# Performance work log

Measured on AMD Instinct MI355X. Metric: run time of the kernel, lower is better.

## Reference

```python
import jax, jax.numpy as jnp
import numpy as np

N, M, E = 14541, 237, 120000
XS, GS, HID, OUT, H = 100, 100, 100, 100, 2
NEG_SLOPE = 0.2


def _l2(v, axis):
    # F.normalize(p=2): x / clamp_min(||x||, 1e-12)
    return v / jnp.maximum(jnp.linalg.norm(v, axis=axis, keepdims=True), 1e-12)


def _rel_att(h_ijk, ends, n, W, b, w_att, out):
    # edge MLP -> [E, H, out]
    c = (h_ijk @ W.T + b).reshape(-1, H, out)
    # attention logits per edge/head, b_ijk = -leaky_relu(a_ijk)
    a = jnp.sum(w_att * c, axis=2, keepdims=True)            # [E, H, 1]
    e = jnp.exp(-jax.nn.leaky_relu(a, NEG_SLOPE))            # [E, H, 1]
    denom = jax.ops.segment_sum(e, ends, num_segments=n)     # [n, H, 1]
    alpha = e / denom[ends]                                  # scatter-softmax
    # self zero-edges in original == segment_sum zero-init; elu(0)=0 matches
    h = jax.ops.segment_sum(alpha * c, ends, num_segments=n) # [n, H, out]
    return jax.nn.elu(h)


def setup_inputs() -> dict:
    key = jax.random.key(0)
    ks = jax.random.split(key, 24)
    f32 = jnp.float32
    def w(k, shp, s=0.1):
        return jax.random.normal(k, shp, dtype=f32) * s
    inp = {
        "x": jax.random.normal(ks[0], (N, XS), dtype=f32),
        "g": jax.random.normal(ks[1], (M, GS), dtype=f32),
        # layer-1 inbound/outbound attention (fc1: [H*HID, 2*XS+GS])
        "W1in": w(ks[2], (H * HID, 2 * XS + GS)), "b1in": jnp.zeros((H * HID,), f32), "a1in": w(ks[3], (1, H, HID)),
        "W1out": w(ks[4], (H * HID, 2 * XS + GS)), "b1out": jnp.zeros((H * HID,), f32), "a1out": w(ks[5], (1, H, HID)),
        "Wa1": w(ks[6], (1, 2 * HID)), "ba1": jnp.zeros((1,), f32),
        # layer-2 attention (fc1: [H*OUT, 2*H*HID+GS])
        "W2in": w(ks[7], (H * OUT, 2 * H * HID + GS)), "b2in": jnp.zeros((H * OUT,), f32), "a2in": w(ks[8], (1, H, OUT)),
        "W2out": w(ks[9], (H * OUT, 2 * H * HID + GS)), "b2out": jnp.zeros((H * OUT,), f32), "a2out": w(ks[10], (1, H, OUT)),
        "Wa2": w(ks[11], (1, 2 * OUT)), "ba2": jnp.zeros((1,), f32),
        # entity residual projection and relation projection
        "Went": w(ks[12], (H * OUT, XS)), "bent": jnp.zeros((H * OUT,), f32),
        "Wrel": w(ks[13], (H * OUT, GS)), "brel": jnp.zeros((H * OUT,), f32),
        "edge_idx": jax.random.randint(ks[14], (2, E), 0, N),
        "edge_type": jax.random.randint(ks[15], (E,), 0, M),
    }
    return inp


def reference(x, g, W1in, b1in, a1in, W1out, b1out, a1out, Wa1, ba1,
              W2in, b2in, a2in, W2out, b2out, a2out, Wa2, ba2,
              Went, bent, Wrel, brel, edge_idx, edge_type):
    n = x.shape[0]
    xn = _l2(x, 1)
    row, col = edge_idx[0], edge_idx[1]
    # layer 1
    h_ijk = jnp.concatenate([xn[row], xn[col], g[edge_type]], axis=1)  # [E, 2*XS+GS]
    hin = _rel_att(h_ijk, col, n, W1in, b1in, a1in, HID)
    hout = _rel_att(h_ijk, row, n, W1out, b1out, a1out, HID)
    al = jax.nn.sigmoid(jnp.concatenate([hin, hout], axis=2) @ Wa1.T + ba1)  # [n, H, 1]
    h = al * hin + (1.0 - al) * hout
    h = _l2(jax.nn.elu(h), 2).reshape(n, H * HID)  # head-concat
    # layer 2
    h_ijk = jnp.concatenate([h[row], h[col], g[edge_type]], axis=1)  # [E, 2*H*HID+GS]
    hin = _rel_att(h_ijk, col, n, W2in, b2in, a2in, OUT)
    hout = _rel_att(h_ijk, row, n, W2out, b2out, a2out, OUT)
    al = jax.nn.sigmoid(jnp.concatenate([hin, hout], axis=2) @ Wa2.T + ba2)
    h = al * hin + (1.0 - al) * hout
    h = _l2(jax.nn.elu(h), 2)                       # [n, H, OUT]
    # entity residual + relation projection
    h_prime = (xn @ Went.T + bent).reshape(n, H, OUT) + h
    h_prime = _l2(h_prime, 2).reshape(n, H * OUT)
    g_prime = g @ Wrel.T + brel                     # [M, H*OUT]
    return h_prime, g_prime
```

## Files before the change

kernel.cpp:

```cpp
#include <hip/hip_runtime.h>
#include <math.h>

#define NSLOPE 0.2f

typedef unsigned short ushort_t;
typedef __attribute__((ext_vector_type(8))) short bf16x8;
typedef __attribute__((ext_vector_type(8))) unsigned short ushort8;
typedef __attribute__((ext_vector_type(4))) float f32x4;

__device__ __forceinline__ float elu1(float x) { return x > 0.f ? x : expm1f(x); }

__device__ __forceinline__ ushort_t f2bf(float f) {
  union { float f; unsigned int u; } v; v.f = f;
  unsigned int r = v.u + 0x7fffu + ((v.u >> 16) & 1u);
  return (ushort_t)(r >> 16);
}
__device__ __forceinline__ float bf2f(ushort_t u) {
  union { unsigned int i; float f; } v; v.i = ((unsigned int)u) << 16; return v.f;
}


__device__ void dev_build_w(int idx,
                            const float* __restrict__ W1in, const float* __restrict__ W1out,
                            const float* __restrict__ W2in, const float* __restrict__ W2out,
                            const float* __restrict__ Went,
                            ushort_t* __restrict__ wcat1, ushort_t* __restrict__ wcat2,
                            ushort_t* __restrict__ wentb) {
  const int S1 = 832 * 128, S2 = 832 * 256, S3 = 256 * 128;
  if (idx < S1) {
    int ro = idx >> 7, k = idx & 127;
    float val = 0.f;
    if (ro < 800 && k < 100) {
      int o = ro / 200, cc = ro - o * 200;
      const float* W = (o < 2) ? W1in : W1out;
      val = W[(size_t)cc * 300 + (o & 1) * 100 + k];
    }
    wcat1[idx] = f2bf(val);
  } else if (idx < S1 + S2) {
    int i2 = idx - S1;
    int ro = i2 >> 8, k = i2 & 255;
    float val = 0.f;
    if (ro < 800 && k < 200) {
      int o = ro / 200, cc = ro - o * 200;
      const float* W = (o < 2) ? W2in : W2out;
      val = W[(size_t)cc * 500 + (o & 1) * 200 + k];
    }
    wcat2[i2] = f2bf(val);
  } else if (idx < S1 + S2 + S3) {
    int i3 = idx - S1 - S2;
    int ro = i3 >> 7, k = i3 & 127;
    float val = (ro < 200 && k < 100) ? Went[ro * 100 + k] : 0.f;
    wentb[i3] = f2bf(val);
  }
}

__device__ void dev_makeu(int idx,
                          const float* __restrict__ W1in, const float* __restrict__ a1in,
                          const float* __restrict__ W1out, const float* __restrict__ a1out,
                          const float* __restrict__ W2in, const float* __restrict__ a2in,
                          const float* __restrict__ W2out, const float* __restrict__ a2out,
                          float* __restrict__ u1in, float* __restrict__ u1out,
                          float* __restrict__ u2in, float* __restrict__ u2out) {
  if (idx >= 3200) return;
  const float* W; const float* avec; float* u; int Kp, local;
  if (idx < 600)       { W = W1in;  avec = a1in;  u = u1in;  Kp = 300; local = idx; }
  else if (idx < 1200) { W = W1out; avec = a1out; u = u1out; Kp = 300; local = idx - 600; }
  else if (idx < 2200) { W = W2in;  avec = a2in;  u = u2in;  Kp = 500; local = idx - 1200; }
  else                 { W = W2out; avec = a2out; u = u2out; Kp = 500; local = idx - 2200; }
  int h = local / Kp, kp = local - h * Kp;
  const float* Wb = W + (size_t)(h * 100) * Kp + kp;
  const float* ab = avec + h * 100;
  float s = 0.f;
  for (int k = 0; k < 100; ++k) s += ab[k] * Wb[(size_t)k * Kp];
  u[local] = s;
}

__device__ void dev_l2norm_q(int bb, int tid, const float* __restrict__ x,
                             ushort_t* __restrict__ xnb,
                             const float* __restrict__ u1in, const float* __restrict__ u1out,
                             float* __restrict__ qA, float* __restrict__ qB,
                             float* __restrict__ qC, float* __restrict__ qD, int N) {
  int wid = bb * 4 + (tid >> 6);
  int lane = tid & 63;
  if (wid >= N) return;
  const float* p = x + (size_t)wid * 100;
  float v0 = p[lane];
  bool t2 = lane < 36;
  float v1 = t2 ? p[lane + 64] : 0.f;
  float ss = v0 * v0 + v1 * v1;
#pragma unroll
  for (int m = 1; m < 64; m <<= 1) ss += __shfl_xor(ss, m, 64);
  float inv = 1.f / fmaxf(sqrtf(ss), 1e-12f);
  float a0 = v0 * inv, a1 = v1 * inv;
  ushort_t* ob = xnb + (size_t)wid * 128;
  ob[lane] = f2bf(a0);
  ob[64 + lane] = t2 ? f2bf(a1) : (ushort_t)0;
  int k0 = lane, k1 = 64 + lane;
  float s[8];
  s[0] = a0 * u1in[k0]        + (t2 ? a1 * u1in[k1]        : 0.f);
  s[1] = a0 * u1in[300 + k0]  + (t2 ? a1 * u1in[300 + k1]  : 0.f);
  s[2] = a0 * u1in[100 + k0]  + (t2 ? a1 * u1in[100 + k1]  : 0.f);
  s[3] = a0 * u1in[400 + k0]  + (t2 ? a1 * u1in[400 + k1]  : 0.f);
  s[4] = a0 * u1out[k0]       + (t2 ? a1 * u1out[k1]       : 0.f);
  s[5] = a0 * u1out[300 + k0] + (t2 ? a1 * u1out[300 + k1] : 0.f);
  s[6] = a0 * u1out[100 + k0] + (t2 ? a1 * u1out[100 + k1] : 0.f);
  s[7] = a0 * u1out[400 + k0] + (t2 ? a1 * u1out[400 + k1] : 0.f);
#pragma unroll
  for (int m = 1; m < 64; m <<= 1) {
#pragma unroll
    for (int i = 0; i < 8; ++i) s[i] += __shfl_xor(s[i], m, 64);
  }
  if (lane == 0) {
    qA[wid * 2] = s[0]; qA[wid * 2 + 1] = s[1];
    qB[wid * 2] = s[2]; qB[wid * 2 + 1] = s[3];
    qC[wid * 2] = s[4]; qC[wid * 2 + 1] = s[5];
    qD[wid * 2] = s[6]; qD[wid * 2 + 1] = s[7];
  }
}

__device__ void dev_qrel2(int bb, int tid, const float* __restrict__ g,
                          const float* __restrict__ u1in, const float* __restrict__ u1out,
                          const float* __restrict__ u2in, const float* __restrict__ u2out,
                          float* __restrict__ q3i1, float* __restrict__ q3o1,
                          float* __restrict__ q3i2, float* __restrict__ q3o2, int Mn) {
  int wid = bb * 4 + (tid >> 6);
  int lane = tid & 63;
  if (wid >= 2 * Mn) return;
  int lay = wid >= Mn;
  int m = wid - lay * Mn;
  const float* uin  = lay ? u2in  : u1in;
  const float* uout = lay ? u2out : u1out;
  int Kp = lay ? 500 : 300;
  int off3 = lay ? 400 : 200;
  float* q3i = lay ? q3i2 : q3i1;
  float* q3o = lay ? q3o2 : q3o1;
  const float* a = g + (size_t)m * 100;
  float s[4] = {0.f, 0.f, 0.f, 0.f};
  for (int k = lane; k < 100; k += 64) {
    float av = a[k];
    s[0] += av * uin[off3 + k];
    s[1] += av * uin[Kp + off3 + k];
    s[2] += av * uout[off3 + k];
    s[3] += av * uout[Kp + off3 + k];
  }
#pragma unroll
  for (int mm = 1; mm < 64; mm <<= 1) {
#pragma unroll
    for (int i = 0; i < 4; ++i) s[i] += __shfl_xor(s[i], mm, 64);
  }
  if (lane == 0) {
    q3i[m * 2] = s[0]; q3i[m * 2 + 1] = s[1];
    q3o[m * 2] = s[2]; q3o[m * 2 + 1] = s[3];
  }
}

__device__ void dev_count(int bb, int tid, const int* __restrict__ row,
                          const int* __restrict__ col,
                          int* __restrict__ cntIn, int* __restrict__ cntOut, int E) {
  int e = bb * 256 + tid;
  if (e >= E) return;
  atomicAdd(&cntIn[col[e]], 1);
  atomicAdd(&cntOut[row[e]], 1);
}

__device__ void dev_edge_e(int bb, int tid,
                           const int* __restrict__ row, const int* __restrict__ col,
                           const int* __restrict__ ety,
                           const float* __restrict__ qA, const float* __restrict__ qB,
                           const float* __restrict__ q3i,
                           const float* __restrict__ qC, const float* __restrict__ qD,
                           const float* __restrict__ q3o,
                           const int* __restrict__ invIn, const int* __restrict__ invOut,
                           float2* __restrict__ eIc, float2* __restrict__ eOc, int E) {
  int e = bb * 256 + tid;
  if (e >= E) return;
  int r = row[e], c = col[e], t = ety[e];
  float2 vA = *(const float2*)(qA + (size_t)r * 2);
  float2 vB = *(const float2*)(qB + (size_t)c * 2);
  float2 v3 = *(const float2*)(q3i + (size_t)t * 2);
  float2 vC = *(const float2*)(qC + (size_t)r * 2);
  float2 vD = *(const float2*)(qD + (size_t)c * 2);
  float2 v4 = *(const float2*)(q3o + (size_t)t * 2);
  float a0 = vA.x + vB.x + v3.x, a1 = vA.y + vB.y + v3.y;
  float b0 = vC.x + vD.x + v4.x, b1 = vC.y + vD.y + v4.y;
  float2 rI, rO;
  rI.x = expf(-(a0 > 0.f ? a0 : NSLOPE * a0));
  rI.y = expf(-(a1 > 0.f ? a1 : NSLOPE * a1));
  rO.x = expf(-(b0 > 0.f ? b0 : NSLOPE * b0));
  rO.y = expf(-(b1 > 0.f ? b1 : NSLOPE * b1));
  eIc[invIn[e]] = rI;
  eOc[invOut[e]] = rO;
}

__device__ void dev_mfma(int bx, int by, int tid,
                         ushort_t* __restrict__ smA, ushort_t* __restrict__ smB,
                         const ushort_t* __restrict__ Ab, int lda,
                         const ushort_t* __restrict__ Bb, int Kpad,
                         int R, int NC, int OUTW, const float* __restrict__ bias,
                         float* __restrict__ C0,
                         ushort_t* __restrict__ Bd0, ushort_t* __restrict__ Bd1,
                         ushort_t* __restrict__ Bd2, ushort_t* __restrict__ Bd3) {
  const int lane = tid & 63;
  const int w = tid >> 6;
  const int wm = w >> 1, wn = w & 1;
  const int m0 = by * 64;
  const int n0 = bx * 64;
  const int srow = tid >> 2;
  const int sq = tid & 3;
  const int sw3 = srow & 7;
  const int sbase = srow * 64;
  const int so0 = sbase + ((((sq << 1) + 0) ^ sw3) << 3);
  const int so1 = sbase + ((((sq << 1) + 1) ^ sw3) << 3);
  const bool aok = (m0 + srow) < R;
  const ushort_t* Ag = Ab + (size_t)(m0 + srow) * lda + sq * 16;
  const ushort_t* Bg = Bb + (size_t)(n0 + srow) * Kpad + sq * 16;
  const int lswz = lane & 7;
  const int hi = lane >> 4;
  const int rA0 = (wm * 32 + (lane & 15)) * 64;
  const int rB0 = (wn * 32 + (lane & 15)) * 64;
  f32x4 acc[2][2] = {};
  for (int k0 = 0; k0 < Kpad; k0 += 64) {
    ushort8 a0 = {0, 0, 0, 0, 0, 0, 0, 0}, a1 = {0, 0, 0, 0, 0, 0, 0, 0};
    if (aok) {
      a0 = *(const ushort8*)(Ag + k0);
      a1 = *(const ushort8*)(Ag + k0 + 8);
    }
    ushort8 b0 = *(const ushort8*)(Bg + k0);
    ushort8 b1 = *(const ushort8*)(Bg + k0 + 8);
    __syncthreads();
    *(ushort8*)(smA + so0) = a0;
    *(ushort8*)(smA + so1) = a1;
    *(ushort8*)(smB + so0) = b0;
    *(ushort8*)(smB + so1) = b1;
    __syncthreads();
#pragma unroll
    for (int ks = 0; ks < 2; ++ks) {
      int co = (((ks << 2) + hi) ^ lswz) << 3;
      bf16x8 aA = *(const bf16x8*)(smA + rA0 + co);
      bf16x8 aB = *(const bf16x8*)(smA + rA0 + 1024 + co);
      bf16x8 bA = *(const bf16x8*)(smB + rB0 + co);
      bf16x8 bB = *(const bf16x8*)(smB + rB0 + 1024 + co);
      acc[0][0] = __builtin_amdgcn_mfma_f32_16x16x32_bf16(aA, bA, acc[0][0], 0, 0, 0);
      acc[0][1] = __builtin_amdgcn_mfma_f32_16x16x32_bf16(aA, bB, acc[0][1], 0, 0, 0);
      acc[1][0] = __builtin_amdgcn_mfma_f32_16x16x32_bf16(aB, bA, acc[1][0], 0, 0, 0);
      acc[1][1] = __builtin_amdgcn_mfma_f32_16x16x32_bf16(aB, bB, acc[1][1], 0, 0, 0);
    }
  }
  ushort_t* Bds[4] = {Bd0, Bd1, Bd2, Bd3};
#pragma unroll
  for (int mt = 0; mt < 2; ++mt) {
    int rr0 = m0 + wm * 32 + mt * 16 + (lane >> 4) * 4;
#pragma unroll
    for (int nt = 0; nt < 2; ++nt) {
      int cc = n0 + wn * 32 + nt * 16 + (lane & 15);
      if (cc < NC) {
        int o = cc / OUTW;
        int c2 = cc - o * OUTW;
        float bv = bias ? bias[c2] : 0.f;
        ushort_t* Bd = Bds[o];
        if (Bd) {
#pragma unroll
          for (int reg = 0; reg < 4; ++reg) {
            int r = rr0 + reg;
            if (r < R) Bd[(size_t)r * OUTW + c2] = f2bf(acc[mt][nt][reg] + bv);
          }
        } else {
#pragma unroll
          for (int reg = 0; reg < 4; ++reg) {
            int r = rr0 + reg;
            if (r < R) C0[(size_t)r * OUTW + c2] = acc[mt][nt][reg] + bv;
          }
        }
      }
    }
  }
}

template <int NOUT, int BF>
__device__ void dev_gemm_multi(int bx, int by, int tid, float4 (*As)[25],
                               const float* __restrict__ A, int lda,
                               const float* __restrict__ W0, const float* __restrict__ W1,
                               int ldw,
                               const float* __restrict__ b0, const float* __restrict__ b1,
                               void* __restrict__ C0v, void* __restrict__ C1v, int R) {
  const int K4 = 25;
  int row0 = by * 32;
  {
    int r = tid >> 3;
    int rr = row0 + r;
    const float4* Ar = (const float4*)(A + (size_t)rr * lda);
    for (int k4 = (tid & 7); k4 < K4; k4 += 8)
      As[r][k4] = (rr < R) ? Ar[k4] : make_float4(0.f, 0.f, 0.f, 0.f);
  }
  __syncthreads();
  int c = bx * 64 + (tid & 63);
  if (c < 200) {
    int rb = (tid >> 6) << 3;
    const float4* Wr[NOUT];
    Wr[0] = (const float4*)(W0 + (size_t)c * ldw);
    if (NOUT > 1) Wr[1] = (const float4*)(W1 + (size_t)c * ldw);
    float acc[NOUT][8];
#pragma unroll
    for (int o = 0; o < NOUT; ++o)
#pragma unroll
      for (int i = 0; i < 8; ++i) acc[o][i] = 0.f;
#pragma unroll 2
    for (int k4 = 0; k4 < K4; ++k4) {
      float4 a[8];
#pragma unroll
      for (int i = 0; i < 8; ++i) a[i] = As[rb + i][k4];
#pragma unroll
      for (int o = 0; o < NOUT; ++o) {
        float4 wv = Wr[o][k4];
#pragma unroll
        for (int i = 0; i < 8; ++i)
          acc[o][i] += a[i].x * wv.x + a[i].y * wv.y + a[i].z * wv.z + a[i].w * wv.w;
      }
    }
    float bv[NOUT];
    bv[0] = b0 ? b0[c] : 0.f;
    if (NOUT > 1) bv[1] = b1 ? b1[c] : 0.f;
    void* Cp[NOUT];
    Cp[0] = C0v;
    if (NOUT > 1) Cp[1] = C1v;
#pragma unroll
    for (int i = 0; i < 8; ++i) {
      int rr = row0 + rb + i;
      if (rr < R) {
#pragma unroll
        for (int o = 0; o < NOUT; ++o) {
          float val = acc[o][i] + bv[o];
          if (BF) ((ushort_t*)Cp[o])[(size_t)rr * 200 + c] = f2bf(val);
          else    ((float*)Cp[o])[(size_t)rr * 200 + c] = val;
        }
      }
    }
  }
}


__global__ __launch_bounds__(256) void MEGA0(
    const float* W1in, const float* W1out, const float* W2in, const float* W2out,
    const float* Went,
    ushort_t* wcat1, ushort_t* wcat2, ushort_t* wentb,
    const float* a1in, const float* a1out, const float* a2in, const float* a2out,
    float* u1in, float* u1out, float* u2in, float* u2out,
    int* cntIn, int* cntOut, int N, int nb_bw, int nb_mk) {
  int b = blockIdx.x, tid = threadIdx.x;
  if (b < nb_bw) {
    dev_build_w(b * 256 + tid, W1in, W1out, W2in, W2out, Went, wcat1, wcat2, wentb);
  } else if (b < nb_bw + nb_mk) {
    dev_makeu((b - nb_bw) * 256 + tid, W1in, a1in, W1out, a1out, W2in, a2in, W2out, a2out,
              u1in, u1out, u2in, u2out);
  } else {
    int idx = (b - nb_bw - nb_mk) * 256 + tid;
    if (idx < N) cntIn[idx] = 0;
    else if (idx < 2 * N) cntOut[idx - N] = 0;
  }
}

__global__ __launch_bounds__(256) void MEGA1(
    const float* x, ushort_t* xnb, const float* u1in, const float* u1out,
    float* qA, float* qB, float* qC, float* qD, int N,
    const float* g, const float* u2in, const float* u2out,
    float* q3i1, float* q3o1, float* q3i2, float* q3o2, int Mn,
    const int* row, const int* col, int* cntIn, int* cntOut, int E,
    int nb_l2, int nb_qr) {
  int b = blockIdx.x, tid = threadIdx.x;
  if (b < nb_l2) {
    dev_l2norm_q(b, tid, x, xnb, u1in, u1out, qA, qB, qC, qD, N);
  } else if (b < nb_l2 + nb_qr) {
    dev_qrel2(b - nb_l2, tid, g, u1in, u1out, u2in, u2out, q3i1, q3o1, q3i2, q3o2, Mn);
  } else {
    dev_count(b - nb_l2 - nb_qr, tid, row, col, cntIn, cntOut, E);
  }
}

__global__ __launch_bounds__(256) void k_scanA(const int* __restrict__ cntIn,
                                               const int* __restrict__ cntOut,
                                               int* __restrict__ part, int N, int nbc) {
  __shared__ int wsum[4];
  int b = blockIdx.x;
  const int* cnt = (b < nbc) ? cntIn : cntOut;
  int cb = (b < nbc) ? b : b - nbc;
  int idx = cb * 256 + threadIdx.x;
  int v = (idx < N) ? cnt[idx] : 0;
#pragma unroll
  for (int m = 1; m < 64; m <<= 1) v += __shfl_xor(v, m, 64);
  if ((threadIdx.x & 63) == 0) wsum[threadIdx.x >> 6] = v;
  __syncthreads();
  if (threadIdx.x == 0) part[b] = wsum[0] + wsum[1] + wsum[2] + wsum[3];
}

__global__ __launch_bounds__(256) void k_scanB(int* __restrict__ part,
                                               int* __restrict__ rsIn, int* __restrict__ rsOut,
                                               int nbc, int N) {
  __shared__ int buf[512];
  int t = threadIdx.x;
  buf[t]       = (t < nbc) ? part[t] : 0;
  buf[256 + t] = (t < nbc) ? part[nbc + t] : 0;
  __syncthreads();
  for (int off = 1; off < 256; off <<= 1) {
    int v0 = (t >= off) ? buf[t - off] : 0;
    int v1 = (t >= off) ? buf[256 + t - off] : 0;
    __syncthreads();
    buf[t] += v0; buf[256 + t] += v1;
    __syncthreads();
  }
  if (t < nbc) {
    part[t]       = (t == 0) ? 0 : buf[t - 1];
    part[nbc + t] = (t == 0) ? 0 : buf[256 + t - 1];
  }
  if (t == 0) { rsIn[N] = buf[nbc - 1]; rsOut[N] = buf[256 + nbc - 1]; }
}

__global__ __launch_bounds__(256) void k_scanC(const int* __restrict__ cntIn,
                                               const int* __restrict__ cntOut,
                                               const int* __restrict__ part,
                                               int* __restrict__ rsIn, int* __restrict__ rsOut,
                                               int* __restrict__ posIn, int* __restrict__ posOut,
                                               int N, int nbc) {
  __shared__ int buf[256];
  int b = blockIdx.x;
  const int* cnt = (b < nbc) ? cntIn : cntOut;
  int* rs  = (b < nbc) ? rsIn : rsOut;
  int* pos = (b < nbc) ? posIn : posOut;
  int cb = (b < nbc) ? b : b - nbc;
  int base = part[b];
  int t = threadIdx.x;
  int idx = cb * 256 + t;
  buf[t] = (idx < N) ? cnt[idx] : 0;
  __syncthreads();
  for (int off = 1; off < 256; off <<= 1) {
    int v = (t >= off) ? buf[t - off] : 0;
    __syncthreads();
    buf[t] += v;
    __syncthreads();
  }
  if (idx < N) {
    int excl = base + ((t == 0) ? 0 : buf[t - 1]);
    rs[idx] = excl; pos[idx] = excl;
  }
}

__global__ void k_fill(const int* __restrict__ row, const int* __restrict__ col,
                       const int* __restrict__ ety,
                       int* __restrict__ posIn, int* __restrict__ posOut,
                       int2* __restrict__ pinIn, int2* __restrict__ pinOut,
                       int* __restrict__ invIn, int* __restrict__ invOut, int E) {
  int e = blockIdx.x * blockDim.x + threadIdx.x;
  if (e >= E) return;
  int r = row[e], c = col[e], tt = ety[e];
  int p = atomicAdd(&posIn[c], 1);
  pinIn[p] = make_int2(r, tt);
  invIn[e] = p;
  int q = atomicAdd(&posOut[r], 1);
  pinOut[q] = make_int2(c, tt);
  invOut[e] = q;
}

__global__ __launch_bounds__(256) void MEGA2(
    const ushort_t* xnb, const ushort_t* wcat1,
    ushort_t* PAb, ushort_t* PBb, ushort_t* PCb, ushort_t* PDb, int N,
    const int* row, const int* col, const int* ety,
    const float* qA, const float* qB, const float* q3i1,
    const float* qC, const float* qD, const float* q3o1,
    const int* invIn, const int* invOut, float2* eIc, float2* eOc, int E,
    const float* g, const float* W1in200, const float* W1out200,
    const float* b1in, const float* b1out, ushort_t* P3ib, ushort_t* P3ob, int Mn,
    const ushort_t* wentb, const float* bent, float* hent,
    const float* Wrel, const float* brel, float* outg,
    int nb_mf, int nb_ee, int nb_gm, int nb_we) {
  __shared__ float4 shbuf4[1024];
  ushort_t* smA = (ushort_t*)shbuf4;
  ushort_t* smB = smA + 64 * 64;
  float4 (*As)[25] = (float4(*)[25])shbuf4;
  int b = blockIdx.x, tid = threadIdx.x;
  if (b < nb_mf) {
    dev_mfma(b % 13, b / 13, tid, smA, smB, xnb, 128, wcat1, 128, N, 800, 200, nullptr,
             nullptr, PAb, PBb, PCb, PDb);
  } else if ((b -= nb_mf) < nb_ee) {
    dev_edge_e(b, tid, row, col, ety, qA, qB, q3i1, qC, qD, q3o1,
               invIn, invOut, eIc, eOc, E);
  } else if ((b -= nb_ee) < nb_gm) {
    dev_gemm_multi<2, 1>(b & 3, b >> 2, tid, As, g, 100, W1in200, W1out200, 300,
                         b1in, b1out, P3ib, P3ob, Mn);
  } else if ((b -= nb_gm) < nb_we) {
    dev_mfma(b & 3, b >> 2, tid, smA, smB, xnb, 128, wentb, 128, N, 200, 200, bent,
             hent, nullptr, nullptr, nullptr, nullptr);
  } else {
    b -= nb_we;
    dev_gemm_multi<1, 0>(b & 3, b >> 2, tid, As, g, 100, Wrel, nullptr, 100,
                         brel, nullptr, outg, nullptr, Mn);
  }
}

__global__ __launch_bounds__(256) void MEGA3(
    const ushort_t* h1b, const ushort_t* wcat2,
    ushort_t* PAb, ushort_t* PBb, ushort_t* PCb, ushort_t* PDb, int N,
    const int* row, const int* col, const int* ety,
    const float* qA, const float* qB, const float* q3i2,
    const float* qC, const float* qD, const float* q3o2,
    const int* invIn, const int* invOut, float2* eIc, float2* eOc, int E,
    const float* g, const float* W2in400, const float* W2out400,
    const float* b2in, const float* b2out, ushort_t* P3ib, ushort_t* P3ob, int Mn,
    int nb_mf, int nb_ee) {
  __shared__ float4 shbuf4[1024];
  ushort_t* smA = (ushort_t*)shbuf4;
  ushort_t* smB = smA + 64 * 64;
  float4 (*As)[25] = (float4(*)[25])shbuf4;
  int b = blockIdx.x, tid = threadIdx.x;
  if (b < nb_mf) {
    dev_mfma(b % 13, b / 13, tid, smA, smB, h1b, 256, wcat2, 256, N, 800, 200, nullptr,
             nullptr, PAb, PBb, PCb, PDb);
  } else if ((b -= nb_mf) < nb_ee) {
    dev_edge_e(b, tid, row, col, ety, qA, qB, q3i2, qC, qD, q3o2,
               invIn, invOut, eIc, eOc, E);
  } else {
    b -= nb_ee;
    dev_gemm_multi<2, 1>(b & 3, b >> 2, tid, As, g, 100, W2in400, W2out400, 500,
                         b2in, b2out, P3ib, P3ob, Mn);
  }
}

__global__ void k_node_att(const int2* __restrict__ pinIn, const float2* __restrict__ eIc,
                           const int* __restrict__ rsIn,
                           const int2* __restrict__ pinOut, const float2* __restrict__ eOc,
                           const int* __restrict__ rsOut,
                           const ushort_t* __restrict__ PAb, const ushort_t* __restrict__ PBb,
                           const ushort_t* __restrict__ PCb, const ushort_t* __restrict__ PDb,
                           const ushort_t* __restrict__ P3ib, const ushort_t* __restrict__ P3ob,
                           const float* __restrict__ Wg, const float* __restrict__ bg,
                           const float* __restrict__ u2in, const float* __restrict__ u2out,
                           float* __restrict__ qA, float* __restrict__ qB,
                           float* __restrict__ qC, float* __restrict__ qD,
                           ushort_t* __restrict__ Hb,
                           const float* __restrict__ hent, float* __restrict__ outp, int N) {
  int wid  = (int)((blockIdx.x * (unsigned)blockDim.x + threadIdx.x) >> 6);
  int lane = threadIdx.x & 63;
  if (wid >= N) return;
  int n = wid;
  int half = lane >> 5, i = lane & 31;
  bool act = i < 25;
  int j = half * 100 + i * 4;
  int sIn = rsIn[n], degIn = rsIn[n + 1] - sIn;
  int sOut = rsOut[n], degOut = rsOut[n + 1] - sOut;
  float4 accIn = {0.f, 0.f, 0.f, 0.f}, accOut = {0.f, 0.f, 0.f, 0.f};
  float dI0 = 0.f, dI1 = 0.f, dO0 = 0.f, dO1 = 0.f;
  int mx = max(degIn, degOut);
  for (int b = 0; b < mx; b += 64) {
    int l = b + lane;
    float2 evI = {0.f, 0.f}, evO = {0.f, 0.f};
    int2 ptI = {0, 0}, ptO = {0, 0};
    if (l < degIn)  { evI = eIc[sIn + l];  ptI = pinIn[sIn + l]; }
    if (l < degOut) { evO = eOc[sOut + l]; ptO = pinOut[sOut + l]; }
    dI0 += evI.x; dI1 += evI.y; dO0 += evO.x; dO1 += evO.y;
    int mI = degIn - b;  if (mI > 64) mI = 64;
    int mO = degOut - b; if (mO > 64) mO = 64;
    int m2 = max(mI, mO);
    for (int jj = 0; jj < m2; ++jj) {
      float aI0 = __shfl(evI.x, jj, 64), aI1 = __shfl(evI.y, jj, 64);
      int rI = __shfl(ptI.x, jj, 64), tI = __shfl(ptI.y, jj, 64);
      float aO0 = __shfl(evO.x, jj, 64), aO1 = __shfl(evO.y, jj, 64);
      int rO = __shfl(ptO.x, jj, 64), tO = __shfl(ptO.y, jj, 64);
      if (act && jj < mI) {
        float wgt = half ? aI1 : aI0;
        ushort4 pa = *(const ushort4*)(PAb + (size_t)rI * 200 + j);
        ushort4 p3 = *(const ushort4*)(P3ib + (size_t)tI * 200 + j);
        accIn.x += wgt * (bf2f(pa.x) + bf2f(p3.x));
        accIn.y += wgt * (bf2f(pa.y) + bf2f(p3.y));
        accIn.z += wgt * (bf2f(pa.z) + bf2f(p3.z));
        accIn.w += wgt * (bf2f(pa.w) + bf2f(p3.w));
      }
      if (act && jj < mO) {
        float wgt = half ? aO1 : aO0;
        ushort4 pd = *(const ushort4*)(PDb + (size_t)rO * 200 + j);
        ushort4 p3 = *(const ushort4*)(P3ob + (size_t)tO * 200 + j);
        accOut.x += wgt * (bf2f(pd.x) + bf2f(p3.x));
        accOut.y += wgt * (bf2f(pd.y) + bf2f(p3.y));
        accOut.z += wgt * (bf2f(pd.z) + bf2f(p3.z));
        accOut.w += wgt * (bf2f(pd.w) + bf2f(p3.w));
      }
    }
  }
#pragma unroll
  for (int m = 1; m < 64; m <<= 1) {
    dI0 += __shfl_xor(dI0, m, 64); dI1 += __shfl_xor(dI1, m, 64);
    dO0 += __shfl_xor(dO0, m, 64); dO1 += __shfl_xor(dO1, m, 64);
  }
  float4 hin = {0.f, 0.f, 0.f, 0.f}, hout = {0.f, 0.f, 0.f, 0.f};
  if (degIn > 0 && act) {
    float invd = 1.f / (half ? dI1 : dI0);
    ushort4 ps = *(const ushort4*)(PBb + (size_t)n * 200 + j);
    hin.x = elu1(bf2f(ps.x) + accIn.x * invd);
    hin.y = elu1(bf2f(ps.y) + accIn.y * invd);
    hin.z = elu1(bf2f(ps.z) + accIn.z * invd);
    hin.w = elu1(bf2f(ps.w) + accIn.w * invd);
  }
  if (degOut > 0 && act) {
    float invd = 1.f / (half ? dO1 : dO0);
    ushort4 ps = *(const ushort4*)(PCb + (size_t)n * 200 + j);
    hout.x = elu1(bf2f(ps.x) + accOut.x * invd);
    hout.y = elu1(bf2f(ps.y) + accOut.y * invd);
    hout.z = elu1(bf2f(ps.z) + accOut.z * invd);
    hout.w = elu1(bf2f(ps.w) + accOut.w * invd);
  }
  float gp = 0.f;
  if (act) {
    int k = i * 4;
    gp = Wg[k] * hin.x + Wg[k + 1] * hin.y + Wg[k + 2] * hin.z + Wg[k + 3] * hin.w +
         Wg[100 + k] * hout.x + Wg[100 + k + 1] * hout.y +
         Wg[100 + k + 2] * hout.z + Wg[100 + k + 3] * hout.w;
  }
#pragma unroll
  for (int m = 1; m < 32; m <<= 1) gp += __shfl_xor(gp, m, 32);
  float al = 1.f / (1.f + expf(-(gp + bg[0])));
  float4 he;
  he.x = elu1(al * hin.x + (1.f - al) * hout.x);
  he.y = elu1(al * hin.y + (1.f - al) * hout.y);
  he.z = elu1(al * hin.z + (1.f - al) * hout.z);
  he.w = elu1(al * hin.w + (1.f - al) * hout.w);
  float ss = he.x * he.x + he.y * he.y + he.z * he.z + he.w * he.w;
#pragma unroll
  for (int m = 1; m < 32; m <<= 1) ss += __shfl_xor(ss, m, 32);
  float inv = 1.f / fmaxf(sqrtf(ss), 1e-12f);
  float4 o = {he.x * inv, he.y * inv, he.z * inv, he.w * inv};
  if (Hb) {
    if (act) {
      ushort4 ov; ov.x = f2bf(o.x); ov.y = f2bf(o.y); ov.z = f2bf(o.z); ov.w = f2bf(o.w);
      *(ushort4*)(Hb + (size_t)n * 256 + j) = ov;
    } else {
      int pi = half * 7 + (i - 25);
      ushort4 z = {0, 0, 0, 0};
      *(ushort4*)(Hb + (size_t)n * 256 + 200 + pi * 4) = z;
    }
  }
  if (outp) {
    float4 v = {0.f, 0.f, 0.f, 0.f};
    if (act) {
      float4 hv = *(const float4*)(hent + (size_t)n * 200 + j);
      v.x = hv.x + o.x; v.y = hv.y + o.y; v.z = hv.z + o.z; v.w = hv.w + o.w;
    }
    float s2 = v.x * v.x + v.y * v.y + v.z * v.z + v.w * v.w;
#pragma unroll
    for (int m = 1; m < 32; m <<= 1) s2 += __shfl_xor(s2, m, 32);
    float inv2 = 1.f / fmaxf(sqrtf(s2), 1e-12f);
    if (act) {
      float4 ov = {v.x * inv2, v.y * inv2, v.z * inv2, v.w * inv2};
      *(float4*)(outp + (size_t)n * 200 + j) = ov;
    }
  }
  if (u2in) {
    float4 ov = act ? o : make_float4(0.f, 0.f, 0.f, 0.f);
    float s[8];
#pragma unroll
    for (int h = 0; h < 2; ++h) {
      float4 uA = *(const float4*)(u2in + h * 500 + j);
      float4 uB = *(const float4*)(u2in + h * 500 + 200 + j);
      float4 uC = *(const float4*)(u2out + h * 500 + j);
      float4 uD = *(const float4*)(u2out + h * 500 + 200 + j);
      s[0 + h] = ov.x * uA.x + ov.y * uA.y + ov.z * uA.z + ov.w * uA.w;
      s[2 + h] = ov.x * uB.x + ov.y * uB.y + ov.z * uB.z + ov.w * uB.w;
      s[4 + h] = ov.x * uC.x + ov.y * uC.y + ov.z * uC.z + ov.w * uC.w;
      s[6 + h] = ov.x * uD.x + ov.y * uD.y + ov.z * uD.z + ov.w * uD.w;
    }
#pragma unroll
    for (int m = 1; m < 64; m <<= 1) {
#pragma unroll
      for (int ii = 0; ii < 8; ++ii) s[ii] += __shfl_xor(s[ii], m, 64);
    }
    if (lane == 0) {
      qA[n * 2] = s[0]; qA[n * 2 + 1] = s[1];
      qB[n * 2] = s[2]; qB[n * 2 + 1] = s[3];
      qC[n * 2] = s[4]; qC[n * 2 + 1] = s[5];
      qD[n * 2] = s[6]; qD[n * 2 + 1] = s[7];
    }
  }
}

extern "C" void kernel_launch(void* const* d_in, const int* in_sizes, int n_in,
                              void* d_out, int out_size, void* d_ws, size_t ws_size,
                              hipStream_t stream) {
  const float* x    = (const float*)d_in[0];
  const float* g    = (const float*)d_in[1];
  const float* W1in = (const float*)d_in[2];
  const float* b1in = (const float*)d_in[3];
  const float* a1in = (const float*)d_in[4];
  const float* W1out= (const float*)d_in[5];
  const float* b1out= (const float*)d_in[6];
  const float* a1out= (const float*)d_in[7];
  const float* Wa1  = (const float*)d_in[8];
  const float* ba1  = (const float*)d_in[9];
  const float* W2in = (const float*)d_in[10];
  const float* b2in = (const float*)d_in[11];
  const float* a2in = (const float*)d_in[12];
  const float* W2out= (const float*)d_in[13];
  const float* b2out= (const float*)d_in[14];
  const float* a2out= (const float*)d_in[15];
  const float* Wa2  = (const float*)d_in[16];
  const float* ba2  = (const float*)d_in[17];
  const float* Went = (const float*)d_in[18];
  const float* bent = (const float*)d_in[19];
  const float* Wrel = (const float*)d_in[20];
  const float* brel = (const float*)d_in[21];
  const int*  eidx  = (const int*)d_in[22];
  const int*  ety   = (const int*)d_in[23];

  const int N = in_sizes[0] / 100;
  const int M = in_sizes[1] / 100;
  const int E = in_sizes[23];
  const int* row = eidx;
  const int* col = eidx + E;
  float* out = (float*)d_out;

  float* ws = (float*)d_ws;
  size_t off = 0;
  auto alloc = [&](size_t nf) { float* p = ws + off; off += (nf + 3) & ~(size_t)3; return p; };
  ushort_t* PAb = (ushort_t*)alloc((size_t)N * 100);
  ushort_t* PBb = (ushort_t*)alloc((size_t)N * 100);
  ushort_t* PCb = (ushort_t*)alloc((size_t)N * 100);
  ushort_t* PDb = (ushort_t*)alloc((size_t)N * 100);
  ushort_t* P3ib = (ushort_t*)alloc((size_t)M * 100);
  ushort_t* P3ob = (ushort_t*)alloc((size_t)M * 100);
  ushort_t* xnb = (ushort_t*)alloc((size_t)N * 64);
  ushort_t* h1b = (ushort_t*)alloc((size_t)N * 128);
  ushort_t* wcat1 = (ushort_t*)alloc((size_t)832 * 64);
  ushort_t* wcat2 = (ushort_t*)alloc((size_t)832 * 128);
  ushort_t* wentb = (ushort_t*)alloc((size_t)256 * 64);
  float* qA  = alloc((size_t)N * 2);
  float* qB  = alloc((size_t)N * 2);
  float* qC  = alloc((size_t)N * 2);
  float* qD  = alloc((size_t)N * 2);
  float* q3i1 = alloc((size_t)M * 2);
  float* q3o1 = alloc((size_t)M * 2);
  float* q3i2 = alloc((size_t)M * 2);
  float* q3o2 = alloc((size_t)M * 2);
  float2* eIc = (float2*)alloc((size_t)E * 2);
  float2* eOc = (float2*)alloc((size_t)E * 2);
  int2* pinIn  = (int2*)alloc((size_t)E * 2);
  int2* pinOut = (int2*)alloc((size_t)E * 2);
  int* invIn  = (int*)alloc((size_t)E);
  int* invOut = (int*)alloc((size_t)E);
  float* hent = alloc((size_t)N * 200);
  float* u1in  = alloc(600);
  float* u1out = alloc(600);
  float* u2in  = alloc(1000);
  float* u2out = alloc(1000);
  int* cntIn  = (int*)alloc((size_t)N);
  int* cntOut = (int*)alloc((size_t)N);
  int* rsIn   = (int*)alloc((size_t)N + 1);
  int* rsOut  = (int*)alloc((size_t)N + 1);
  int* posIn  = (int*)alloc((size_t)N);
  int* posOut = (int*)alloc((size_t)N);
  int* part   = (int*)alloc((size_t)512);

  const int gN4 = (N + 3) / 4;
  const int gE  = (E + 255) / 256;
  const int mT  = (N + 63) / 64;
  const int nbc = (N + 255) / 256;

  const int nb_bw = (832 * 128 + 832 * 256 + 256 * 128 + 255) / 256;
  const int nb_mk = 13;
  const int nb_z  = (2 * N + 255) / 256;
  const int nb_l2 = gN4;
  const int nb_qr = (2 * M + 3) / 4;
  const int nb_mf = 13 * mT;
  const int nb_gm = 4 * ((M + 31) / 32);
  const int nb_we = 4 * mT;

  MEGA0<<<nb_bw + nb_mk + nb_z, 256, 0, stream>>>(
      W1in, W1out, W2in, W2out, Went, wcat1, wcat2, wentb,
      a1in, a1out, a2in, a2out, u1in, u1out, u2in, u2out,
      cntIn, cntOut, N, nb_bw, nb_mk);

  MEGA1<<<nb_l2 + nb_qr + gE, 256, 0, stream>>>(
      x, xnb, u1in, u1out, qA, qB, qC, qD, N,
      g, u2in, u2out, q3i1, q3o1, q3i2, q3o2, M,
      row, col, cntIn, cntOut, E, nb_l2, nb_qr);

  k_scanA<<<2 * nbc, 256, 0, stream>>>(cntIn, cntOut, part, N, nbc);
  k_scanB<<<1, 256, 0, stream>>>(part, rsIn, rsOut, nbc, N);
  k_scanC<<<2 * nbc, 256, 0, stream>>>(cntIn, cntOut, part, rsIn, rsOut, posIn, posOut, N, nbc);
  k_fill<<<gE, 256, 0, stream>>>(row, col, ety, posIn, posOut, pinIn, pinOut, invIn, invOut, E);

  MEGA2<<<nb_mf + gE + nb_gm + nb_we + nb_gm, 256, 0, stream>>>(
      xnb, wcat1, PAb, PBb, PCb, PDb, N,
      row, col, ety, qA, qB, q3i1, qC, qD, q3o1, invIn, invOut, eIc, eOc, E,
      g, W1in + 200, W1out + 200, b1in, b1out, P3ib, P3ob, M,
      wentb, bent, hent, Wrel, brel, out + (size_t)N * 200,
      nb_mf, gE, nb_gm, nb_we);

  k_node_att<<<gN4, 256, 0, stream>>>(pinIn, eIc, rsIn, pinOut, eOc, rsOut,
                                      PAb, PBb, PCb, PDb, P3ib, P3ob, Wa1, ba1,
                                      u2in, u2out, qA, qB, qC, qD,
                                      h1b, nullptr, nullptr, N);

  MEGA3<<<nb_mf + gE + nb_gm, 256, 0, stream>>>(
      h1b, wcat2, PAb, PBb, PCb, PDb, N,
      row, col, ety, qA, qB, q3i2, qC, qD, q3o2, invIn, invOut, eIc, eOc, E,
      g, W2in + 400, W2out + 400, b2in, b2out, P3ib, P3ob, M,
      nb_mf, gE);

  k_node_att<<<gN4, 256, 0, stream>>>(pinIn, eIc, rsIn, pinOut, eOc, rsOut,
                                      PAb, PBb, PCb, PDb, P3ib, P3ob, Wa2, ba2,
                                      nullptr, nullptr, qA, qB, qC, qD,
                                      nullptr, hent, out, N);
}
```

Measured before the change: 200.3 us.

## Pack edge weights with CSR indices, stage them in LDS, move layer-2 relation GEMM earlier

Edge exp-weights and CSR (neighbor, type) pairs now share one interleaved float4 record per edge. The node-attention kernel reads a single 16-byte record per edge and stages records in shared memory, replacing eight wave shuffles per neighbor. The layer-2 relation GEMM moves into the earlier mega-kernel so MEGA3 holds only MFMA and edge work. The entity residual projection is stored as bf16 instead of fp32, halving that traffic at some cost in precision.

```diff
diff --git a/kernel.cpp b/kernel.cpp
--- a/kernel.cpp
+++ b/kernel.cpp
@@ -171,7 +171,7 @@
                            const float* __restrict__ qC, const float* __restrict__ qD,
                            const float* __restrict__ q3o,
                            const int* __restrict__ invIn, const int* __restrict__ invOut,
-                           float2* __restrict__ eIc, float2* __restrict__ eOc, int E) {
+                           float4* __restrict__ recI, float4* __restrict__ recO, int E) {
   int e = bb * 256 + tid;
   if (e >= E) return;
   int r = row[e], c = col[e], t = ety[e];
@@ -188,8 +188,8 @@
   rI.y = expf(-(a1 > 0.f ? a1 : NSLOPE * a1));
   rO.x = expf(-(b0 > 0.f ? b0 : NSLOPE * b0));
   rO.y = expf(-(b1 > 0.f ? b1 : NSLOPE * b1));
-  eIc[invIn[e]] = rI;
-  eOc[invOut[e]] = rO;
+  *(float2*)(recI + invIn[e]) = rI;
+  *(float2*)(recO + invOut[e]) = rO;
 }
 
 __device__ void dev_mfma(int bx, int by, int tid,
@@ -446,16 +446,16 @@
 __global__ void k_fill(const int* __restrict__ row, const int* __restrict__ col,
                        const int* __restrict__ ety,
                        int* __restrict__ posIn, int* __restrict__ posOut,
-                       int2* __restrict__ pinIn, int2* __restrict__ pinOut,
+                       float4* __restrict__ recI, float4* __restrict__ recO,
                        int* __restrict__ invIn, int* __restrict__ invOut, int E) {
   int e = blockIdx.x * blockDim.x + threadIdx.x;
   if (e >= E) return;
   int r = row[e], c = col[e], tt = ety[e];
   int p = atomicAdd(&posIn[c], 1);
-  pinIn[p] = make_int2(r, tt);
+  ((int2*)(recI + p))[1] = make_int2(r, tt);
   invIn[e] = p;
   int q = atomicAdd(&posOut[r], 1);
-  pinOut[q] = make_int2(c, tt);
+  ((int2*)(recO + q))[1] = make_int2(c, tt);
   invOut[e] = q;
 }
 
@@ -465,10 +465,12 @@
     const int* row, const int* col, const int* ety,
     const float* qA, const float* qB, const float* q3i1,
     const float* qC, const float* qD, const float* q3o1,
-    const int* invIn, const int* invOut, float2* eIc, float2* eOc, int E,
+    const int* invIn, const int* invOut, float4* recI, float4* recO, int E,
     const float* g, const float* W1in200, const float* W1out200,
-    const float* b1in, const float* b1out, ushort_t* P3ib, ushort_t* P3ob, int Mn,
-    const ushort_t* wentb, const float* bent, float* hent,
+    const float* b1in, const float* b1out, ushort_t* P3ib, ushort_t* P3ob,
+    const float* W2in400, const float* W2out400,
+    const float* b2in, const float* b2out, ushort_t* P3ib2, ushort_t* P3ob2, int Mn,
+    const ushort_t* wentb, const float* bent, ushort_t* hentb,
     const float* Wrel, const float* brel, float* outg,
     int nb_mf, int nb_ee, int nb_gm, int nb_we) {
   __shared__ float4 shbuf4[1024];
@@ -481,13 +483,16 @@
              nullptr, PAb, PBb, PCb, PDb);
   } else if ((b -= nb_mf) < nb_ee) {
     dev_edge_e(b, tid, row, col, ety, qA, qB, q3i1, qC, qD, q3o1,
-               invIn, invOut, eIc, eOc, E);
+               invIn, invOut, recI, recO, E);
   } else if ((b -= nb_ee) < nb_gm) {
     dev_gemm_multi<2, 1>(b & 3, b >> 2, tid, As, g, 100, W1in200, W1out200, 300,
                          b1in, b1out, P3ib, P3ob, Mn);
+  } else if ((b -= nb_gm) < nb_gm) {
+    dev_gemm_multi<2, 1>(b & 3, b >> 2, tid, As, g, 100, W2in400, W2out400, 500,
+                         b2in, b2out, P3ib2, P3ob2, Mn);
   } else if ((b -= nb_gm) < nb_we) {
     dev_mfma(b & 3, b >> 2, tid, smA, smB, xnb, 128, wentb, 128, N, 200, 200, bent,
-             hent, nullptr, nullptr, nullptr, nullptr);
+             nullptr, hentb, nullptr, nullptr, nullptr);
   } else {
     b -= nb_we;
     dev_gemm_multi<1, 0>(b & 3, b >> 2, tid, As, g, 100, Wrel, nullptr, 100,
@@ -501,32 +506,23 @@
     const int* row, const int* col, const int* ety,
     const float* qA, const float* qB, const float* q3i2,
     const float* qC, const float* qD, const float* q3o2,
-    const int* invIn, const int* invOut, float2* eIc, float2* eOc, int E,
-    const float* g, const float* W2in400, const float* W2out400,
-    const float* b2in, const float* b2out, ushort_t* P3ib, ushort_t* P3ob, int Mn,
-    int nb_mf, int nb_ee) {
+    const int* invIn, const int* invOut, float4* recI, float4* recO, int E,
+    int nb_mf) {
   __shared__ float4 shbuf4[1024];
   ushort_t* smA = (ushort_t*)shbuf4;
   ushort_t* smB = smA + 64 * 64;
-  float4 (*As)[25] = (float4(*)[25])shbuf4;
   int b = blockIdx.x, tid = threadIdx.x;
   if (b < nb_mf) {
     dev_mfma(b % 13, b / 13, tid, smA, smB, h1b, 256, wcat2, 256, N, 800, 200, nullptr,
              nullptr, PAb, PBb, PCb, PDb);
-  } else if ((b -= nb_mf) < nb_ee) {
-    dev_edge_e(b, tid, row, col, ety, qA, qB, q3i2, qC, qD, q3o2,
-               invIn, invOut, eIc, eOc, E);
   } else {
-    b -= nb_ee;
-    dev_gemm_multi<2, 1>(b & 3, b >> 2, tid, As, g, 100, W2in400, W2out400, 500,
-                         b2in, b2out, P3ib, P3ob, Mn);
-  }
-}
-
-__global__ void k_node_att(const int2* __restrict__ pinIn, const float2* __restrict__ eIc,
-                           const int* __restrict__ rsIn,
-                           const int2* __restrict__ pinOut, const float2* __restrict__ eOc,
-                           const int* __restrict__ rsOut,
+    dev_edge_e(b - nb_mf, tid, row, col, ety, qA, qB, q3i2, qC, qD, q3o2,
+               invIn, invOut, recI, recO, E);
+  }
+}
+
+__global__ void k_node_att(const float4* __restrict__ recI, const int* __restrict__ rsIn,
+                           const float4* __restrict__ recO, const int* __restrict__ rsOut,
                            const ushort_t* __restrict__ PAb, const ushort_t* __restrict__ PBb,
                            const ushort_t* __restrict__ PCb, const ushort_t* __restrict__ PDb,
                            const ushort_t* __restrict__ P3ib, const ushort_t* __restrict__ P3ob,
@@ -535,7 +531,10 @@
                            float* __restrict__ qA, float* __restrict__ qB,
                            float* __restrict__ qC, float* __restrict__ qD,
                            ushort_t* __restrict__ Hb,
-                           const float* __restrict__ hent, float* __restrict__ outp, int N) {
+                           const ushort_t* __restrict__ hentb, float* __restrict__ outp, int N) {
+  __shared__ float4 sRecI[4][64];
+  __shared__ float4 sRecO[4][64];
+  int wv = threadIdx.x >> 6;
   int wid  = (int)((blockIdx.x * (unsigned)blockDim.x + threadIdx.x) >> 6);
   int lane = threadIdx.x & 63;
   if (wid >= N) return;
@@ -550,21 +549,24 @@
   int mx = max(degIn, degOut);
   for (int b = 0; b < mx; b += 64) {
     int l = b + lane;
-    float2 evI = {0.f, 0.f}, evO = {0.f, 0.f};
-    int2 ptI = {0, 0}, ptO = {0, 0};
-    if (l < degIn)  { evI = eIc[sIn + l];  ptI = pinIn[sIn + l]; }
-    if (l < degOut) { evO = eOc[sOut + l]; ptO = pinOut[sOut + l]; }
-    dI0 += evI.x; dI1 += evI.y; dO0 += evO.x; dO1 += evO.y;
+    if (l < degIn) {
+      float4 rc = recI[sIn + l];
+      dI0 += rc.x; dI1 += rc.y;
+      sRecI[wv][lane] = rc;
+    }
+    if (l < degOut) {
+      float4 rc = recO[sOut + l];
+      dO0 += rc.x; dO1 += rc.y;
+      sRecO[wv][lane] = rc;
+    }
     int mI = degIn - b;  if (mI > 64) mI = 64;
     int mO = degOut - b; if (mO > 64) mO = 64;
     int m2 = max(mI, mO);
     for (int jj = 0; jj < m2; ++jj) {
-      float aI0 = __shfl(evI.x, jj, 64), aI1 = __shfl(evI.y, jj, 64);
-      int rI = __shfl(ptI.x, jj, 64), tI = __shfl(ptI.y, jj, 64);
-      float aO0 = __shfl(evO.x, jj, 64), aO1 = __shfl(evO.y, jj, 64);
-      int rO = __shfl(ptO.x, jj, 64), tO = __shfl(ptO.y, jj, 64);
       if (act && jj < mI) {
-        float wgt = half ? aI1 : aI0;
+        float4 rc = sRecI[wv][jj];
+        int rI = __float_as_int(rc.z), tI = __float_as_int(rc.w);
+        float wgt = half ? rc.y : rc.x;
         ushort4 pa = *(const ushort4*)(PAb + (size_t)rI * 200 + j);
         ushort4 p3 = *(const ushort4*)(P3ib + (size_t)tI * 200 + j);
         accIn.x += wgt * (bf2f(pa.x) + bf2f(p3.x));
@@ -573,7 +575,9 @@
         accIn.w += wgt * (bf2f(pa.w) + bf2f(p3.w));
       }
       if (act && jj < mO) {
-        float wgt = half ? aO1 : aO0;
+        float4 rc = sRecO[wv][jj];
+        int rO = __float_as_int(rc.z), tO = __float_as_int(rc.w);
+        float wgt = half ? rc.y : rc.x;
         ushort4 pd = *(const ushort4*)(PDb + (size_t)rO * 200 + j);
         ushort4 p3 = *(const ushort4*)(P3ob + (size_t)tO * 200 + j);
         accOut.x += wgt * (bf2f(pd.x) + bf2f(p3.x));
@@ -638,8 +642,9 @@
   if (outp) {
     float4 v = {0.f, 0.f, 0.f, 0.f};
     if (act) {
-      float4 hv = *(const float4*)(hent + (size_t)n * 200 + j);
-      v.x = hv.x + o.x; v.y = hv.y + o.y; v.z = hv.z + o.z; v.w = hv.w + o.w;
+      ushort4 hv = *(const ushort4*)(hentb + (size_t)n * 200 + j);
+      v.x = bf2f(hv.x) + o.x; v.y = bf2f(hv.y) + o.y;
+      v.z = bf2f(hv.z) + o.z; v.w = bf2f(hv.w) + o.w;
     }
     float s2 = v.x * v.x + v.y * v.y + v.z * v.z + v.w * v.w;
 #pragma unroll
@@ -716,14 +721,19 @@
   float* ws = (float*)d_ws;
   size_t off = 0;
   auto alloc = [&](size_t nf) { float* p = ws + off; off += (nf + 3) & ~(size_t)3; return p; };
+  float4* recI = (float4*)alloc((size_t)E * 4);
+  float4* recO = (float4*)alloc((size_t)E * 4);
   ushort_t* PAb = (ushort_t*)alloc((size_t)N * 100);
   ushort_t* PBb = (ushort_t*)alloc((size_t)N * 100);
   ushort_t* PCb = (ushort_t*)alloc((size_t)N * 100);
   ushort_t* PDb = (ushort_t*)alloc((size_t)N * 100);
   ushort_t* P3ib = (ushort_t*)alloc((size_t)M * 100);
   ushort_t* P3ob = (ushort_t*)alloc((size_t)M * 100);
+  ushort_t* P3ib2 = (ushort_t*)alloc((size_t)M * 100);
+  ushort_t* P3ob2 = (ushort_t*)alloc((size_t)M * 100);
   ushort_t* xnb = (ushort_t*)alloc((size_t)N * 64);
   ushort_t* h1b = (ushort_t*)alloc((size_t)N * 128);
+  ushort_t* hentb = (ushort_t*)alloc((size_t)N * 100);
   ushort_t* wcat1 = (ushort_t*)alloc((size_t)832 * 64);
   ushort_t* wcat2 = (ushort_t*)alloc((size_t)832 * 128);
   ushort_t* wentb = (ushort_t*)alloc((size_t)256 * 64);
@@ -735,13 +745,8 @@
   float* q3o1 = alloc((size_t)M * 2);
   float* q3i2 = alloc((size_t)M * 2);
   float* q3o2 = alloc((size_t)M * 2);
-  float2* eIc = (float2*)alloc((size_t)E * 2);
-  float2* eOc = (float2*)alloc((size_t)E * 2);
-  int2* pinIn  = (int2*)alloc((size_t)E * 2);
-  int2* pinOut = (int2*)alloc((size_t)E * 2);
   int* invIn  = (int*)alloc((size_t)E);
   int* invOut = (int*)alloc((size_t)E);
-  float* hent = alloc((size_t)N * 200);
   float* u1in  = alloc(600);
   float* u1out = alloc(600);
   float* u2in  = alloc(1000);
@@ -781,28 +786,28 @@
   k_scanA<<<2 * nbc, 256, 0, stream>>>(cntIn, cntOut, part, N, nbc);
   k_scanB<<<1, 256, 0, stream>>>(part, rsIn, rsOut, nbc, N);
   k_scanC<<<2 * nbc, 256, 0, stream>>>(cntIn, cntOut, part, rsIn, rsOut, posIn, posOut, N, nbc);
-  k_fill<<<gE, 256, 0, stream>>>(row, col, ety, posIn, posOut, pinIn, pinOut, invIn, invOut, E);
-
-  MEGA2<<<nb_mf + gE + nb_gm + nb_we + nb_gm, 256, 0, stream>>>(
+  k_fill<<<gE, 256, 0, stream>>>(row, col, ety, posIn, posOut, recI, recO, invIn, invOut, E);
+
+  MEGA2<<<nb_mf + gE + nb_gm * 3 + nb_we, 256, 0, stream>>>(
       xnb, wcat1, PAb, PBb, PCb, PDb, N,
-      row, col, ety, qA, qB, q3i1, qC, qD, q3o1, invIn, invOut, eIc, eOc, E,
-      g, W1in + 200, W1out + 200, b1in, b1out, P3ib, P3ob, M,
-      wentb, bent, hent, Wrel, brel, out + (size_t)N * 200,
+      row, col, ety, qA, qB, q3i1, qC, qD, q3o1, invIn, invOut, recI, recO, E,
+      g, W1in + 200, W1out + 200, b1in, b1out, P3ib, P3ob,
+      W2in + 400, W2out + 400, b2in, b2out, P3ib2, P3ob2, M,
+      wentb, bent, hentb, Wrel, brel, out + (size_t)N * 200,
       nb_mf, gE, nb_gm, nb_we);
 
-  k_node_att<<<gN4, 256, 0, stream>>>(pinIn, eIc, rsIn, pinOut, eOc, rsOut,
+  k_node_att<<<gN4, 256, 0, stream>>>(recI, rsIn, recO, rsOut,
                                       PAb, PBb, PCb, PDb, P3ib, P3ob, Wa1, ba1,
                                       u2in, u2out, qA, qB, qC, qD,
                                       h1b, nullptr, nullptr, N);
 
-  MEGA3<<<nb_mf + gE + nb_gm, 256, 0, stream>>>(
+  MEGA3<<<nb_mf + gE, 256, 0, stream>>>(
       h1b, wcat2, PAb, PBb, PCb, PDb, N,
-      row, col, ety, qA, qB, q3i2, qC, qD, q3o2, invIn, invOut, eIc, eOc, E,
-      g, W2in + 400, W2out + 400, b2in, b2out, P3ib, P3ob, M,
-      nb_mf, gE);
-
-  k_node_att<<<gN4, 256, 0, stream>>>(pinIn, eIc, rsIn, pinOut, eOc, rsOut,
-                                      PAb, PBb, PCb, PDb, P3ib, P3ob, Wa2, ba2,
+      row, col, ety, qA, qB, q3i2, qC, qD, q3o2, invIn, invOut, recI, recO, E,
+      nb_mf);
+
+  k_node_att<<<gN4, 256, 0, stream>>>(recI, rsIn, recO, rsOut,
+                                      PAb, PBb, PCb, PDb, P3ib2, P3ob2, Wa2, ba2,
                                       nullptr, nullptr, qA, qB, qC, qD,
-                                      nullptr, hent, out, N);
-}
+                                      nullptr, hentb, out, N);
+}
```

Result: faster. 186.6 us (-6.8%).
